# Kernel optimization log

Measured on AMD Instinct MI355X. Metric: run time of the kernel, lower is better.

The kernel has to match this reference:

```python
import jax, jax.numpy as jnp
import numpy as np
import math

RANKS = [16, 8, 4, 2, 1]          # generate_mrlora_ranks(32 // 2)
LORA_ALPHA = 16.0
SCALES = [LORA_ALPHA / math.sqrt(r) for r in RANKS]  # use_rslora=True
D_IN = 4096
D_OUT = 4096


def setup_inputs() -> dict:
    key = jax.random.key(0)
    ks = jax.random.split(key, 3 + 2 * len(RANKS))
    x = jax.random.normal(ks[0], (4, 2048, D_IN), dtype=jnp.float32)
    W = jax.random.normal(ks[1], (D_OUT, D_IN), dtype=jnp.float32) * (1.0 / math.sqrt(D_IN))
    b = jax.random.normal(ks[2], (D_OUT,), dtype=jnp.float32) * 0.01
    inp = {"x": x, "W": W, "b": b}
    for i, r in enumerate(RANKS):
        # A: [r, D_IN], B: [D_OUT, r] (torch nn.Linear weight layout)
        inp[f"A{r}"] = jax.random.normal(ks[3 + 2 * i], (r, D_IN), dtype=jnp.float32) * (1.0 / math.sqrt(D_IN))
        inp[f"B{r}"] = jax.random.normal(ks[4 + 2 * i], (D_OUT, r), dtype=jnp.float32) * 0.02
    inp["alphas"] = jnp.ones((len(RANKS),), dtype=jnp.float32)
    return inp


def reference(x, W, b, A16, B16, A8, B8, A4, B4, A2, B2, A1, B1, alphas):
    # base linear: x @ W.T + b
    out = jnp.einsum('bsd,od->bso', x, W) + b
    As = [A16, A8, A4, A2, A1]
    Bs = [B16, B8, B4, B2, B1]
    # dropout p=0 -> identity; per-rank low-rank update with learned + rslora scale
    for i, (A, B) in enumerate(zip(As, Bs)):
        coef = alphas[i] * SCALES[i]
        out = out + coef * jnp.einsum('bsr,or->bso', jnp.einsum('bsd,rd->bsr', x, A), B)
    return out
```

## Files before the change

kernel.cpp:

```cpp
#include <hip/hip_runtime.h>
#include <hip/hip_bf16.h>
#include <stdint.h>

#define DK 4096
#define MROWS 8192
#define NOUT 4096
#define KP 4160
#define KP_B (KP*2)
#define NT 65

typedef __attribute__((ext_vector_type(8))) __bf16 bf16x8;
typedef __attribute__((ext_vector_type(4))) float f32x4;
typedef unsigned short u16;

struct __align__(8) us4 { u16 x, y, z, w; };

__device__ __forceinline__ u16 f2bf(float f) {
  union { float f; uint32_t u; } v; v.f = f;
  uint32_t r = v.u + 0x7fffu + ((v.u >> 16) & 1u);
  return (u16)(r >> 16);
}

__device__ __forceinline__ void gload16(const void* g, void* l) {
  __builtin_amdgcn_global_load_lds(
      (const __attribute__((address_space(1))) unsigned int*)g,
      (__attribute__((address_space(3))) unsigned int*)l, 16, 0, 0);
}

__global__ void conv_x(const float* __restrict__ x, u16* __restrict__ xb) {
  int m = blockIdx.x, t = threadIdx.x;
  const float* src = x + (size_t)m * DK;
  u16* dst = xb + (size_t)m * KP;
#pragma unroll
  for (int j = 0; j < 4; ++j) {
    int col = (t + j * 256) * 4;
    float4 v = *reinterpret_cast<const float4*>(src + col);
    us4 o = { f2bf(v.x), f2bf(v.y), f2bf(v.z), f2bf(v.w) };
    *reinterpret_cast<us4*>(dst + col) = o;
  }
  if (t < 64) dst[4096 + t] = 0;
}

__global__ void build_W(const float* __restrict__ W,
                        const float* __restrict__ B16, const float* __restrict__ B8,
                        const float* __restrict__ B4,  const float* __restrict__ B2,
                        const float* __restrict__ B1,  const float* __restrict__ alphas,
                        u16* __restrict__ wb) {
  int n = blockIdx.x, t = threadIdx.x;
  const float* src = W + (size_t)n * DK;
  u16* dst = wb + (size_t)n * KP;
#pragma unroll
  for (int j = 0; j < 4; ++j) {
    int col = (t + j * 256) * 4;
    float4 v = *reinterpret_cast<const float4*>(src + col);
    us4 o = { f2bf(v.x), f2bf(v.y), f2bf(v.z), f2bf(v.w) };
    *reinterpret_cast<us4*>(dst + col) = o;
  }
  if (t < 64) {
    u16 val = 0;
    if (t < 31) {
      float coef; const float* Bp; int r, rl;
      if (t < 16)      { coef = alphas[0] * 4.0f;                Bp = B16; r = 16; rl = t; }
      else if (t < 24) { coef = alphas[1] * 5.656854249492381f;  Bp = B8;  r = 8;  rl = t - 16; }
      else if (t < 28) { coef = alphas[2] * 8.0f;                Bp = B4;  r = 4;  rl = t - 24; }
      else if (t < 30) { coef = alphas[3] * 11.313708498984761f; Bp = B2;  r = 2;  rl = t - 28; }
      else             { coef = alphas[4] * 16.0f;               Bp = B1;  r = 1;  rl = 0; }
      val = f2bf(coef * Bp[(size_t)n * r + rl]);
    }
    dst[4096 + t] = val;
  }
}

__global__ void build_A(const float* __restrict__ A16, const float* __restrict__ A8,
                        const float* __restrict__ A4,  const float* __restrict__ A2,
                        const float* __restrict__ A1,  u16* __restrict__ ab) {
  int rr = blockIdx.x, t = threadIdx.x;
  const float* src = nullptr;
  if (rr < 16)      src = A16 + (size_t)rr * DK;
  else if (rr < 24) src = A8 + (size_t)(rr - 16) * DK;
  else if (rr < 28) src = A4 + (size_t)(rr - 24) * DK;
  else if (rr < 30) src = A2 + (size_t)(rr - 28) * DK;
  else if (rr < 31) src = A1;
  u16* dst = ab + (size_t)rr * DK;
#pragma unroll
  for (int j = 0; j < 4; ++j) {
    int col = (t + j * 256) * 4;
    us4 o = { 0, 0, 0, 0 };
    if (src) {
      float4 v = *reinterpret_cast<const float4*>(src + col);
      o = { f2bf(v.x), f2bf(v.y), f2bf(v.z), f2bf(v.w) };
    }
    *reinterpret_cast<us4*>(dst + col) = o;
  }
}

__global__ __launch_bounds__(256, 2) void xa_gemm(u16* xb, const u16* __restrict__ ab) {
  __shared__ u16 Xs[64 * 64];
  __shared__ u16 Qs[32 * 64];
  int m0 = blockIdx.x * 64;
  int t = threadIdx.x, lane = t & 63, w = t >> 6;
  int l15 = lane & 15, lg = lane >> 4;
  f32x4 acc[2] = {};
  const char* xbase = (const char*)xb + (size_t)m0 * KP_B;
  for (int kt = 0; kt < 64; ++kt) {
    size_t kb = (size_t)kt * 128;
    __syncthreads();
#pragma unroll
    for (int i = 0; i < 2; ++i) {
      int chunk = w * 2 + i;
      int off = chunk * 1024 + lane * 16;
      int row = off >> 7, colB = off & 127;
      gload16(xbase + (size_t)row * KP_B + kb + colB, (char*)Xs + chunk * 1024);
    }
    {
      int off = w * 1024 + lane * 16;
      int row = off >> 7, colB = off & 127;
      gload16((const char*)ab + (size_t)row * (DK * 2) + kb + colB, (char*)Qs + w * 1024);
    }
    asm volatile("s_waitcnt vmcnt(0)" ::: "memory");
    __syncthreads();
#pragma unroll
    for (int ks = 0; ks < 2; ++ks) {
      bf16x8 xf = *reinterpret_cast<const bf16x8*>((const char*)Xs + (w * 16 + l15) * 128 + ks * 64 + lg * 16);
#pragma unroll
      for (int ni = 0; ni < 2; ++ni) {
        bf16x8 af = *reinterpret_cast<const bf16x8*>((const char*)Qs + (ni * 16 + l15) * 128 + ks * 64 + lg * 16);
        acc[ni] = __builtin_amdgcn_mfma_f32_16x16x32_bf16(xf, af, acc[ni], 0, 0, 0);
      }
    }
  }
#pragma unroll
  for (int ni = 0; ni < 2; ++ni)
#pragma unroll
    for (int r = 0; r < 4; ++r) {
      int m = m0 + w * 16 + lg * 4 + r;
      int c = 4096 + ni * 16 + l15;
      xb[(size_t)m * KP + c] = f2bf(acc[ni][r]);
    }
}

__device__ __forceinline__ void stage_tile(const char* gbase, char* lbase, int w, int lane, int i) {
  int chunk = (w << 2) + i;
  int row = (chunk << 3) + (lane >> 3);
  int src_c = ((lane & 7) ^ (lane >> 3)) << 4;
  gload16(gbase + (size_t)row * KP_B + src_c, lbase + chunk * 1024);
}

__device__ __forceinline__ bf16x8 rdfrag(const char* base, int row, int cb) {
  return *reinterpret_cast<const bf16x8*>(base + row * 128 + (cb ^ ((row & 7) << 4)));
}

__global__ __launch_bounds__(512, 2) void gemm_main(const u16* __restrict__ xb, const u16* __restrict__ wb,
                                                    const float* __restrict__ bias, float* __restrict__ out) {
  __shared__ u16 As0[256 * 64], As1[256 * 64];
  __shared__ u16 Bs0[256 * 64], Bs1[256 * 64];
  int bid = blockIdx.x;
  int swz = (bid & 7) * 64 + (bid >> 3);
  int mt = swz >> 4, nt = swz & 15;
  int m0 = mt * 256, n0 = nt * 256;
  int t = threadIdx.x, lane = t & 63, w = t >> 6;
  int wr = w >> 2, wc = w & 3;
  int l15 = lane & 15, lg = lane >> 4;

  f32x4 acc[8][4] = {};
  bf16x8 af[4][2], bl[2][2], bh[2][2];

  const char* Ag = (const char*)xb + (size_t)m0 * KP_B;
  const char* Bg = (const char*)wb + (size_t)n0 * KP_B;
  char *AcA = (char*)As0, *AnA = (char*)As1, *AcB = (char*)Bs0, *AnB = (char*)Bs1;

#pragma unroll
  for (int i = 0; i < 4; ++i) stage_tile(Bg, AcB, w, lane, i);
#pragma unroll
  for (int i = 0; i < 4; ++i) stage_tile(Ag, AcA, w, lane, i);
#pragma unroll
  for (int i = 0; i < 4; ++i) stage_tile(Bg + 128, AnB, w, lane, i);
  asm volatile("s_waitcnt vmcnt(4)" ::: "memory");
  __builtin_amdgcn_s_barrier();

  const int Arow = wr * 128 + l15;
  const int Brow = wc * 64 + l15;
  const int cb0 = lg * 16;

  for (int kt = 0; kt < NT; ++kt) {
    const char* Agk1 = Ag + (size_t)(kt + 1) * 128;
    const char* Bgk2 = Bg + (size_t)(kt + 2) * 128;
    const bool doA = (kt + 1 < NT), doB = (kt + 2 < NT);

#pragma unroll
    for (int mi = 0; mi < 4; ++mi)
#pragma unroll
      for (int ks = 0; ks < 2; ++ks)
        af[mi][ks] = rdfrag(AcA, Arow + mi * 16, cb0 + ks * 64);
#pragma unroll
    for (int ni = 0; ni < 2; ++ni)
#pragma unroll
      for (int ks = 0; ks < 2; ++ks)
        bl[ni][ks] = rdfrag(AcB, Brow + ni * 16, cb0 + ks * 64);
    if (doA) { stage_tile(Agk1, AnA, w, lane, 0); stage_tile(Agk1, AnA, w, lane, 1); }
    asm volatile("s_waitcnt lgkmcnt(8)" ::: "memory");
    __builtin_amdgcn_s_barrier();
    asm volatile("s_waitcnt lgkmcnt(0)" ::: "memory");
    __builtin_amdgcn_sched_barrier(0);
    __builtin_amdgcn_s_setprio(1);
#pragma unroll
    for (int mi = 0; mi < 4; ++mi)
#pragma unroll
      for (int ni = 0; ni < 2; ++ni)
#pragma unroll
        for (int ks = 0; ks < 2; ++ks)
          acc[mi][ni] = __builtin_amdgcn_mfma_f32_16x16x32_bf16(af[mi][ks], bl[ni][ks], acc[mi][ni], 0, 0, 0);
    __builtin_amdgcn_s_setprio(0);
    __builtin_amdgcn_s_barrier();

#pragma unroll
    for (int ni = 0; ni < 2; ++ni)
#pragma unroll
      for (int ks = 0; ks < 2; ++ks)
        bh[ni][ks] = rdfrag(AcB, Brow + 32 + ni * 16, cb0 + ks * 64);
    if (doA) { stage_tile(Agk1, AnA, w, lane, 2); stage_tile(Agk1, AnA, w, lane, 3); }
    __builtin_amdgcn_s_barrier();
    asm volatile("s_waitcnt lgkmcnt(0)" ::: "memory");
    __builtin_amdgcn_sched_barrier(0);
    __builtin_amdgcn_s_setprio(1);
#pragma unroll
    for (int mi = 0; mi < 4; ++mi)
#pragma unroll
      for (int ni = 0; ni < 2; ++ni)
#pragma unroll
        for (int ks = 0; ks < 2; ++ks)
          acc[mi][ni + 2] = __builtin_amdgcn_mfma_f32_16x16x32_bf16(af[mi][ks], bh[ni][ks], acc[mi][ni + 2], 0, 0, 0);
    __builtin_amdgcn_s_setprio(0);
    __builtin_amdgcn_s_barrier();

#pragma unroll
    for (int mi = 0; mi < 4; ++mi)
#pragma unroll
      for (int ks = 0; ks < 2; ++ks)
        af[mi][ks] = rdfrag(AcA, Arow + 64 + mi * 16, cb0 + ks * 64);
    if (doB) { stage_tile(Bgk2, AcB, w, lane, 0); stage_tile(Bgk2, AcB, w, lane, 1); }
    __builtin_amdgcn_s_barrier();
    asm volatile("s_waitcnt lgkmcnt(0)" ::: "memory");
    __builtin_amdgcn_sched_barrier(0);
    __builtin_amdgcn_s_setprio(1);
#pragma unroll
    for (int mi = 0; mi < 4; ++mi)
#pragma unroll
      for (int ni = 0; ni < 2; ++ni)
#pragma unroll
        for (int ks = 0; ks < 2; ++ks)
          acc[mi + 4][ni + 2] = __builtin_amdgcn_mfma_f32_16x16x32_bf16(af[mi][ks], bh[ni][ks], acc[mi + 4][ni + 2], 0, 0, 0);
    __builtin_amdgcn_s_setprio(0);
    __builtin_amdgcn_s_barrier();

    if (doB) { stage_tile(Bgk2, AcB, w, lane, 2); stage_tile(Bgk2, AcB, w, lane, 3); }
    __builtin_amdgcn_s_barrier();
    __builtin_amdgcn_s_setprio(1);
#pragma unroll
    for (int mi = 0; mi < 4; ++mi)
#pragma unroll
      for (int ni = 0; ni < 2; ++ni)
#pragma unroll
        for (int ks = 0; ks < 2; ++ks)
          acc[mi + 4][ni] = __builtin_amdgcn_mfma_f32_16x16x32_bf16(af[mi][ks], bl[ni][ks], acc[mi + 4][ni], 0, 0, 0);
    __builtin_amdgcn_s_setprio(0);
    if (kt < NT - 2) asm volatile("s_waitcnt vmcnt(4)" ::: "memory");
    else             asm volatile("s_waitcnt vmcnt(0)" ::: "memory");
    __builtin_amdgcn_s_barrier();

    { char* tp = AcA; AcA = AnA; AnA = tp; }
    { char* tp = AcB; AcB = AnB; AnB = tp; }
  }

  float bn[4];
#pragma unroll
  for (int ni = 0; ni < 4; ++ni) bn[ni] = bias[n0 + wc * 64 + ni * 16 + l15];
#pragma unroll
  for (int mi = 0; mi < 8; ++mi) {
    int mbase = m0 + wr * 128 + mi * 16 + lg * 4;
#pragma unroll
    for (int ni = 0; ni < 4; ++ni) {
      int n = n0 + wc * 64 + ni * 16 + l15;
#pragma unroll
      for (int r = 0; r < 4; ++r)
        out[(size_t)(mbase + r) * NOUT + n] = acc[mi][ni][r] + bn[ni];
    }
  }
}

extern "C" void kernel_launch(void* const* d_in, const int* in_sizes, int n_in,
                              void* d_out, int out_size, void* d_ws, size_t ws_size,
                              hipStream_t stream) {
  const float* x   = (const float*)d_in[0];
  const float* W   = (const float*)d_in[1];
  const float* b   = (const float*)d_in[2];
  const float* A16 = (const float*)d_in[3];
  const float* B16 = (const float*)d_in[4];
  const float* A8  = (const float*)d_in[5];
  const float* B8  = (const float*)d_in[6];
  const float* A4  = (const float*)d_in[7];
  const float* B4  = (const float*)d_in[8];
  const float* A2  = (const float*)d_in[9];
  const float* B2  = (const float*)d_in[10];
  const float* A1  = (const float*)d_in[11];
  const float* B1  = (const float*)d_in[12];
  const float* alphas = (const float*)d_in[13];

  char* ws = (char*)d_ws;
  u16* xb = (u16*)ws;
  u16* wb = (u16*)(ws + 68157440);
  u16* ab = (u16*)(ws + 68157440 + 34078720);
  float* out = (float*)d_out;

  conv_x<<<MROWS, 256, 0, stream>>>(x, xb);
  build_W<<<NOUT, 256, 0, stream>>>(W, B16, B8, B4, B2, B1, alphas, wb);
  build_A<<<32, 256, 0, stream>>>(A16, A8, A4, A2, A1, ab);
  xa_gemm<<<MROWS / 64, 256, 0, stream>>>(xb, ab);
  gemm_main<<<(MROWS / 256) * (NOUT / 256), 512, 0, stream>>>(xb, wb, b, out);
}
```

Measured before the change: 321.0 us.

## Fuse x fp32-to-bf16 conversion into the x·A low-rank projection kernel

Merges the separate conversion kernel and the xa_gemm kernel into one conv_xa kernel. Each block now reads fp32 x, converts it to bf16, writes it to both the padded workspace and a swizzled LDS tile, and computes the rank-32 projection from LDS in the same pass. This removes one full reread of the bf16 x workspace and one kernel launch. In exchange it uses 16-row tiles where only two of four waves issue MFMAs, so compute utilisation in this kernel drops and the block count rises.

```diff
diff --git a/kernel.cpp b/kernel.cpp
--- a/kernel.cpp
+++ b/kernel.cpp
@@ -14,6 +14,7 @@
 typedef unsigned short u16;
 
 struct __align__(8) us4 { u16 x, y, z, w; };
+struct __align__(16) us8 { u16 a[8]; };
 
 __device__ __forceinline__ u16 f2bf(float f) {
   union { float f; uint32_t u; } v; v.f = f;
@@ -27,18 +28,8 @@
       (__attribute__((address_space(3))) unsigned int*)l, 16, 0, 0);
 }
 
-__global__ void conv_x(const float* __restrict__ x, u16* __restrict__ xb) {
-  int m = blockIdx.x, t = threadIdx.x;
-  const float* src = x + (size_t)m * DK;
-  u16* dst = xb + (size_t)m * KP;
-#pragma unroll
-  for (int j = 0; j < 4; ++j) {
-    int col = (t + j * 256) * 4;
-    float4 v = *reinterpret_cast<const float4*>(src + col);
-    us4 o = { f2bf(v.x), f2bf(v.y), f2bf(v.z), f2bf(v.w) };
-    *reinterpret_cast<us4*>(dst + col) = o;
-  }
-  if (t < 64) dst[4096 + t] = 0;
+__device__ __forceinline__ bf16x8 rdfrag(const void* base, int row, int cb) {
+  return *reinterpret_cast<const bf16x8*>((const char*)base + row * 128 + (cb ^ ((row & 7) << 4)));
 }
 
 __global__ void build_W(const float* __restrict__ W,
@@ -94,49 +85,52 @@
   }
 }
 
-__global__ __launch_bounds__(256, 2) void xa_gemm(u16* xb, const u16* __restrict__ ab) {
-  __shared__ u16 Xs[64 * 64];
+__global__ __launch_bounds__(256, 2) void conv_xa(const float* __restrict__ x, u16* __restrict__ xb,
+                                                  const u16* __restrict__ ab) {
+  __shared__ u16 Xs[16 * 64];
   __shared__ u16 Qs[32 * 64];
-  int m0 = blockIdx.x * 64;
+  int m0 = blockIdx.x * 16;
   int t = threadIdx.x, lane = t & 63, w = t >> 6;
   int l15 = lane & 15, lg = lane >> 4;
-  f32x4 acc[2] = {};
-  const char* xbase = (const char*)xb + (size_t)m0 * KP_B;
+  int crow = t >> 4;
+  int cc = (t & 15) * 4;
+  f32x4 acc = {};
+  const float* xp = x + (size_t)(m0 + crow) * DK + cc;
+  u16* xbp = xb + (size_t)(m0 + crow) * KP + cc;
+  char* xsw = (char*)Xs + crow * 128 + ((cc * 2) ^ ((crow & 7) << 4));
+  const char* qsrc = (const char*)ab + (size_t)(t >> 3) * (DK * 2)
+                   + (((t & 7) ^ ((t >> 3) & 7)) << 4);
+  char* qdst = (char*)Qs + t * 16;
+
   for (int kt = 0; kt < 64; ++kt) {
-    size_t kb = (size_t)kt * 128;
+    float4 v = *reinterpret_cast<const float4*>(xp + kt * 64);
+    us4 o = { f2bf(v.x), f2bf(v.y), f2bf(v.z), f2bf(v.w) };
     __syncthreads();
-#pragma unroll
-    for (int i = 0; i < 2; ++i) {
-      int chunk = w * 2 + i;
-      int off = chunk * 1024 + lane * 16;
-      int row = off >> 7, colB = off & 127;
-      gload16(xbase + (size_t)row * KP_B + kb + colB, (char*)Xs + chunk * 1024);
-    }
-    {
-      int off = w * 1024 + lane * 16;
-      int row = off >> 7, colB = off & 127;
-      gload16((const char*)ab + (size_t)row * (DK * 2) + kb + colB, (char*)Qs + w * 1024);
-    }
+    *reinterpret_cast<us4*>(xsw) = o;
+    *reinterpret_cast<us4*>(xbp + kt * 64) = o;
+    gload16(qsrc + (size_t)kt * 128, qdst);
     asm volatile("s_waitcnt vmcnt(0)" ::: "memory");
     __syncthreads();
-#pragma unroll
-    for (int ks = 0; ks < 2; ++ks) {
-      bf16x8 xf = *reinterpret_cast<const bf16x8*>((const char*)Xs + (w * 16 + l15) * 128 + ks * 64 + lg * 16);
-#pragma unroll
-      for (int ni = 0; ni < 2; ++ni) {
-        bf16x8 af = *reinterpret_cast<const bf16x8*>((const char*)Qs + (ni * 16 + l15) * 128 + ks * 64 + lg * 16);
-        acc[ni] = __builtin_amdgcn_mfma_f32_16x16x32_bf16(xf, af, acc[ni], 0, 0, 0);
+    if (w < 2) {
+#pragma unroll
+      for (int ks = 0; ks < 2; ++ks) {
+        bf16x8 xf = rdfrag(Xs, l15, ks * 64 + lg * 16);
+        bf16x8 af = rdfrag(Qs, w * 16 + l15, ks * 64 + lg * 16);
+        acc = __builtin_amdgcn_mfma_f32_16x16x32_bf16(xf, af, acc, 0, 0, 0);
       }
     }
   }
-#pragma unroll
-  for (int ni = 0; ni < 2; ++ni)
+  if (w < 2) {
 #pragma unroll
     for (int r = 0; r < 4; ++r) {
-      int m = m0 + w * 16 + lg * 4 + r;
-      int c = 4096 + ni * 16 + l15;
-      xb[(size_t)m * KP + c] = f2bf(acc[ni][r]);
-    }
+      int m = m0 + lg * 4 + r;
+      xb[(size_t)m * KP + 4096 + w * 16 + l15] = f2bf(acc[r]);
+    }
+  }
+  if (t < 128) {
+    us4 z = { 0, 0, 0, 0 };
+    *reinterpret_cast<us4*>(xb + (size_t)(m0 + (t >> 3)) * KP + 4128 + (t & 7) * 4) = z;
+  }
 }
 
 __device__ __forceinline__ void stage_tile(const char* gbase, char* lbase, int w, int lane, int i) {
@@ -144,10 +138,6 @@
   int row = (chunk << 3) + (lane >> 3);
   int src_c = ((lane & 7) ^ (lane >> 3)) << 4;
   gload16(gbase + (size_t)row * KP_B + src_c, lbase + chunk * 1024);
-}
-
-__device__ __forceinline__ bf16x8 rdfrag(const char* base, int row, int cb) {
-  return *reinterpret_cast<const bf16x8*>(base + row * 128 + (cb ^ ((row & 7) << 4)));
 }
 
 __global__ __launch_bounds__(512, 2) void gemm_main(const u16* __restrict__ xb, const u16* __restrict__ wb,
@@ -312,9 +302,8 @@
   u16* ab = (u16*)(ws + 68157440 + 34078720);
   float* out = (float*)d_out;
 
-  conv_x<<<MROWS, 256, 0, stream>>>(x, xb);
+  build_A<<<32, 256, 0, stream>>>(A16, A8, A4, A2, A1, ab);
   build_W<<<NOUT, 256, 0, stream>>>(W, B16, B8, B4, B2, B1, alphas, wb);
-  build_A<<<32, 256, 0, stream>>>(A16, A8, A4, A2, A1, ab);
-  xa_gemm<<<MROWS / 64, 256, 0, stream>>>(xb, ab);
+  conv_xa<<<MROWS / 16, 256, 0, stream>>>(x, xb, ab);
   gemm_main<<<(MROWS / 256) * (NOUT / 256), 512, 0, stream>>>(xb, wb, b, out);
 }
```

Result: slower. 339.6 us (+5.8%).
